# Kernel tuning notes

Measured on AMD Instinct MI355X. Metric: run time of the kernel, lower is better.

## Reference

```python
import jax, jax.numpy as jnp
import numpy as np

B, M, T, R, N_IN, O, K = 2, 20000, 8, 5, 64, 128, 4  # batch, verts, N_theta, N_rho, in, out, kernels


def setup_inputs() -> dict:
    key = jax.random.key(0)
    k1, k2, k3, k4 = jax.random.split(key, 4)
    signal = jax.random.normal(k1, (B, M, N_IN), dtype=jnp.float32)
    u = jax.random.uniform(k2, (B, M, T, R, 3), dtype=jnp.float32, minval=1e-3, maxval=1.0)
    bary_weights = u / jnp.sum(u, axis=-1, keepdims=True)  # barycentric: sum to 1
    bary_indices = jax.random.randint(k3, (B, M, T, R, 3), 0, M, dtype=jnp.int32)
    # glorot-ish scale for (amt_kernel, N_theta, N_rho, out, in) weight tensor
    kernel = jax.random.normal(k4, (K, T, R, O, N_IN), dtype=jnp.float32) * 0.05
    return {"signal": signal, "bary_weights": bary_weights,
            "bary_indices": bary_indices, "kernel": kernel}


def reference(signal, bary_weights, bary_indices, kernel):
    # signal: (B, m, n); bary_weights/indices: (B, m, T, R, 3); kernel: (K, T, R, o, n)
    Ksum = jnp.sum(kernel, axis=0)                      # sum over kernels k: (T, R, o, n)
    T_ = kernel.shape[1]
    j = jnp.arange(T_)
    rot = (j[None, :] + j[:, None]) % T_                # rot[r, j] = (j + r) % T
    Krot = Ksum[rot]                                    # (T_r, T_j, R, o, n)

    def one(sig, w, idx):
        g = sig[idx]                                    # gather: (m, T, R, 3, n)
        x = jnp.einsum('mtrc,mtrcn->mtrn', w, g)        # barycentric pullback (m, T, R, n)
        conv = jnp.einsum('rjion,mjin->rmo', Krot, x)   # per-rotation conv (T_r, m, o)
        a = jax.nn.relu(conv)
        norms = jnp.linalg.norm(a, axis=-1)             # (T_r, m)
        best = jnp.argmax(norms, axis=0)                # (m,)
        return jnp.take_along_axis(a, best[None, :, None], axis=0)[0]  # angular max pool (m, o)

    return jax.vmap(one)(signal, bary_weights, bary_indices)
```

## Files before the change

### kernel.cpp

```cpp
#include <hip/hip_runtime.h>
#include <hip/hip_bf16.h>


typedef _Float16 f16;
typedef _Float16 f16x8 __attribute__((ext_vector_type(8)));
typedef float f32x4 __attribute__((ext_vector_type(4)));

#define B_   2
#define M_   20000
#define T_   8
#define R_   5
#define NIN  64
#define O_   128
#define K_   4

#define PTS   (B_*M_)
#define KSEG  2560
#define KPHY  5120
#define KLOG  7680
#define NQ    1024
#define SCALE 16.0f
#define INVSS (1.0f/(SCALE*SCALE))

#define BM    64
#define BK    32
#define TS    (KLOG/BK)

__global__ void k_ksum(const float* __restrict__ kern, float* __restrict__ ksum) {
    int i = blockIdx.x * 256 + threadIdx.x;
    const int total = T_ * R_ * O_ * NIN;
    if (i >= total) return;
    float s = 0.f;
#pragma unroll
    for (int k = 0; k < K_; k++) s += kern[k * total + i];
    ksum[i] = s;
}

__global__ void k_wt(const float* __restrict__ ksum, f16* __restrict__ wt) {
    int idx = blockIdx.x * 256 + threadIdx.x;
    const int total = NQ * KSEG;
    if (idx >= total) return;
    int q = idx / KSEG;
    int k = idx - q * KSEG;
    int r = q >> 7, o = q & 127;
    int j = k / 320;
    int rem = k - j * 320;
    int i = rem >> 6, n = rem & 63;
    int t = (j + r) & 7;
    float v = SCALE * ksum[((((t * R_ + i) * O_ + o) << 6) + n)];
    f16 hi = (f16)v;
    f16 lo = (f16)(v - (float)hi);
    f16* row = wt + (size_t)q * KLOG;
    row[k] = hi;
    row[k + KSEG] = hi;
    row[k + 2 * KSEG] = lo;
}

__global__ void k_interp(const float* __restrict__ sig, const float* __restrict__ bw,
                         const int* __restrict__ bi, f16* __restrict__ X,
                         int pt0, int rows_pad) {
    int nwaves = gridDim.x * 4;
    int wav = (blockIdx.x * 256 + threadIdx.x) >> 6;
    int lane = threadIdx.x & 63;
    int ntask = rows_pad * T_;
    for (int task = wav; task < ntask; task += nwaves) {
        int lr = task >> 3;
        int j = task & 7;
        int pt = pt0 + lr;
        f16* rowp = X + (size_t)lr * KPHY + j * 320;
        if (pt >= PTS) {
#pragma unroll
            for (int i = 0; i < R_; i++) {
                rowp[i * 64 + lane] = (f16)0.f;
                rowp[KSEG + i * 64 + lane] = (f16)0.f;
            }
            continue;
        }
        int b = (pt >= M_) ? 1 : 0;
        const float* sb = sig + (size_t)b * M_ * NIN;
        size_t base = (size_t)pt * 120 + j * 15;
        float wv = 0.f;
        int iv = 0;
        if (lane < 15) { wv = bw[base + lane]; iv = bi[base + lane]; }
#pragma unroll
        for (int i = 0; i < R_; i++) {
            float w0 = __shfl(wv, i * 3 + 0, 64);
            float w1 = __shfl(wv, i * 3 + 1, 64);
            float w2 = __shfl(wv, i * 3 + 2, 64);
            int i0 = __shfl(iv, i * 3 + 0, 64);
            int i1 = __shfl(iv, i * 3 + 1, 64);
            int i2 = __shfl(iv, i * 3 + 2, 64);
            float x = w0 * sb[(size_t)i0 * NIN + lane];
            x = fmaf(w1, sb[(size_t)i1 * NIN + lane], x);
            x = fmaf(w2, sb[(size_t)i2 * NIN + lane], x);
            x *= SCALE;
            f16 hi = (f16)x;
            f16 lo = (f16)(x - (float)hi);
            rowp[i * 64 + lane] = hi;
            rowp[KSEG + i * 64 + lane] = lo;
        }
    }
}

__global__ __launch_bounds__(512, 2) void k_gemm_fused(
    const f16* __restrict__ X, const f16* __restrict__ WT,
    float* __restrict__ out, int pt0) {
    __shared__ __align__(16) f16 As[2][64 * 32];
    __shared__ __align__(16) f16 Bs[2][1024 * 32];
    __shared__ float sred[8][64];
    const int m0 = blockIdx.x * BM;
    const int t = threadIdx.x;
    const int w = t >> 6, lane = t & 63;
    const int wr = w >> 2, wc = w & 3;
    const int lq = lane >> 4, lr16 = lane & 15;
    const int flane = (lr16 >> 1) & 3;
    const int src_off = (((lane & 3) ^ ((lane >> 3) & 3)) << 3);

    f32x4 acc[2][16];
#pragma unroll
    for (int a = 0; a < 2; a++)
#pragma unroll
        for (int b = 0; b < 16; b++) acc[a][b] = (f32x4){0.f, 0.f, 0.f, 0.f};

    const f16* pA = X + (size_t)(m0 + 8 * w + ((lane & 31) >> 2)) * KPHY + src_off;
    const f16* pB = WT + (size_t)(w * 128 + (lane >> 2)) * KLOG + src_off;

#define STAGE(S, BUF) do {                                                                \
        int k0_ = (S) * BK;                                                               \
        int kA_ = k0_ - ((k0_ >= KPHY) ? KPHY : 0);               \
        if (lane < 32)                                                                    \
            __builtin_amdgcn_global_load_lds(                                             \
                (const __attribute__((address_space(1))) void*)(pA + kA_),                \
                (__attribute__((address_space(3))) void*)(&As[BUF][w * 256 + (lane & 31) * 8]), \
                16, 0, 0);                                                                \
        _Pragma("unroll")                                                                 \
        for (int i_ = 0; i_ < 8; i_++)                                                    \
            __builtin_amdgcn_global_load_lds(                                             \
                (const __attribute__((address_space(1))) void*)(pB + i_ * 16 * KLOG + k0_), \
                (__attribute__((address_space(3))) void*)(&Bs[BUF][(w * 8 + i_) * 512 + lane * 8]), \
                16, 0, 0);                                                                \
    } while (0)

    STAGE(0, 0);

    for (int s = 0; s < TS; ++s) {
        int cur = s & 1;
        if (s + 1 < TS) {
            STAGE(s + 1, cur ^ 1);
            asm volatile("s_waitcnt vmcnt(9)" ::: "memory");
        } else {
            asm volatile("s_waitcnt vmcnt(0)" ::: "memory");
        }
        __builtin_amdgcn_s_barrier();
        __builtin_amdgcn_sched_barrier(0);

        const f16* Ac = &As[cur][0];
        const f16* Bc = &Bs[cur][0];
        const int cho = (lq ^ flane) << 3;
        f16x8 af0 = *(const f16x8*)(Ac + (wr * 32 + lr16) * 32 + cho);
        f16x8 af1 = *(const f16x8*)(Ac + (wr * 32 + 16 + lr16) * 32 + cho);
#pragma unroll
        for (int nf = 0; nf < 16; nf++) {
            f16x8 bf = *(const f16x8*)(Bc + (wc * 256 + nf * 16 + lr16) * 32 + cho);
            acc[0][nf] = __builtin_amdgcn_mfma_f32_16x16x32_f16(af0, bf, acc[0][nf], 0, 0, 0);
            acc[1][nf] = __builtin_amdgcn_mfma_f32_16x16x32_f16(af1, bf, acc[1][nf], 0, 0, 0);
        }
        __builtin_amdgcn_sched_barrier(0);
        __builtin_amdgcn_s_barrier();
    }
#undef STAGE

#pragma unroll
    for (int mf = 0; mf < 2; mf++)
#pragma unroll
        for (int nf = 0; nf < 16; nf++)
#pragma unroll
            for (int jj = 0; jj < 4; jj++)
                acc[mf][nf][jj] = fmaxf(acc[mf][nf][jj], 0.f);

#pragma unroll
    for (int mf = 0; mf < 2; mf++)
#pragma unroll
        for (int jj = 0; jj < 4; jj++)
#pragma unroll
            for (int half = 0; half < 2; half++) {
                float s = 0.f;
#pragma unroll
                for (int nf2 = 0; nf2 < 8; nf2++) {
                    float v = acc[mf][half * 8 + nf2][jj];
                    s = fmaf(v, v, s);
                }
                s += __shfl_xor(s, 1, 64);
                s += __shfl_xor(s, 2, 64);
                s += __shfl_xor(s, 4, 64);
                s += __shfl_xor(s, 8, 64);
                if (lr16 == 0) sred[wc * 2 + half][wr * 32 + mf * 16 + lq * 4 + jj] = s;
            }
    __syncthreads();

#pragma unroll
    for (int mf = 0; mf < 2; mf++)
#pragma unroll
        for (int jj = 0; jj < 4; jj++) {
            int row = wr * 32 + mf * 16 + lq * 4 + jj;
            float bs = sred[0][row];
            int br = 0;
#pragma unroll
            for (int r = 1; r < 8; r++) {
                float v = sred[r][row];
                if (v > bs) { bs = v; br = r; }
            }
            int pt = pt0 + m0 + row;
            if ((br >> 1) == wc && pt < PTS) {
                float* op = out + (size_t)pt * O_ + lr16;
                if (br & 1) {
#pragma unroll
                    for (int nf2 = 0; nf2 < 8; nf2++) op[nf2 * 16] = acc[mf][8 + nf2][jj] * INVSS;
                } else {
#pragma unroll
                    for (int nf2 = 0; nf2 < 8; nf2++) op[nf2 * 16] = acc[mf][nf2][jj] * INVSS;
                }
            }
        }
}

extern "C" void kernel_launch(void* const* d_in, const int* in_sizes, int n_in,
                              void* d_out, int out_size, void* d_ws, size_t ws_size,
                              hipStream_t stream) {
    const float* sig = (const float*)d_in[0];
    const float* bw = (const float*)d_in[1];
    const int* bi = (const int*)d_in[2];
    const float* kern = (const float*)d_in[3];
    float* out = (float*)d_out;
    char* ws = (char*)d_ws;

    const size_t sz_ksum = (size_t)T_ * R_ * O_ * NIN * sizeof(float);
    const size_t sz_wt = (size_t)NQ * KLOG * sizeof(f16);
    float* ksum = (float*)ws;
    f16* WT = (f16*)(ws + sz_ksum);
    f16* X = (f16*)(ws + sz_ksum + sz_wt);

    size_t persist = sz_ksum + sz_wt;
    size_t avail = (ws_size > persist) ? (ws_size - persist) : 0;
    long maxrows = (long)(avail / ((size_t)KPHY * sizeof(f16)));
    int chunk = (int)((maxrows / BM) * BM);
    if (chunk < BM) chunk = BM;
    const int PTS_PAD = ((PTS + BM - 1) / BM) * BM;
    if (chunk > PTS_PAD) chunk = PTS_PAD;

    k_ksum<<<(T_ * R_ * O_ * NIN + 255) / 256, 256, 0, stream>>>(kern, ksum);
    k_wt<<<(NQ * KSEG + 255) / 256, 256, 0, stream>>>(ksum, WT);

    for (int pt0 = 0; pt0 < PTS; pt0 += chunk) {
        int rem = PTS - pt0;
        int rows = (rem < chunk) ? rem : chunk;
        int rows_pad = (rows + BM - 1) & ~(BM - 1);
        k_interp<<<2048, 256, 0, stream>>>(sig, bw, bi, X, pt0, rows_pad);
        k_gemm_fused<<<rows_pad / BM, 512, 0, stream>>>(X, WT, out, pt0);
    }
}
```

Measured before the change: 1.650 ms.

## Retile GEMM to 256x256 blocks with XCD remap and separate select pass

The fused GEMM previously used 64-row blocks that each covered all 1024 rotation-output columns. It now uses 256x256 tiles with BK=64 and an XCD-aware block remapping. Conv results and per-rotation-pair norms go to global memory, and a new k_select kernel does the argmax and pooled write. This raises arithmetic intensity and reuse of the shared weight operand, at the cost of an extra fp32 conv buffer round-trip and one more launch. The interp kernel also replaces shuffle broadcasts with wave-uniform scalar loads.

```diff
diff --git a/kernel.cpp b/kernel.cpp
--- a/kernel.cpp
+++ b/kernel.cpp
@@ -15,6 +15,7 @@
 #define K_   4
 
 #define PTS   (B_*M_)
+#define PTSPAD 40192
 #define KSEG  2560
 #define KPHY  5120
 #define KLOG  7680
@@ -22,8 +23,8 @@
 #define SCALE 16.0f
 #define INVSS (1.0f/(SCALE*SCALE))
 
-#define BM    64
-#define BK    32
+#define BM    256
+#define BK    64
 #define TS    (KLOG/BK)
 
 __global__ void k_ksum(const float* __restrict__ kern, float* __restrict__ ksum) {
@@ -64,8 +65,9 @@
     int lane = threadIdx.x & 63;
     int ntask = rows_pad * T_;
     for (int task = wav; task < ntask; task += nwaves) {
-        int lr = task >> 3;
-        int j = task & 7;
+        int tu = __builtin_amdgcn_readfirstlane(task);
+        int lr = tu >> 3;
+        int j = tu & 7;
         int pt = pt0 + lr;
         f16* rowp = X + (size_t)lr * KPHY + j * 320;
         if (pt >= PTS) {
@@ -78,18 +80,12 @@
         }
         int b = (pt >= M_) ? 1 : 0;
         const float* sb = sig + (size_t)b * M_ * NIN;
-        size_t base = (size_t)pt * 120 + j * 15;
-        float wv = 0.f;
-        int iv = 0;
-        if (lane < 15) { wv = bw[base + lane]; iv = bi[base + lane]; }
+        const float* wp = bw + (size_t)pt * 120 + j * 15;
+        const int* ip = bi + (size_t)pt * 120 + j * 15;
 #pragma unroll
         for (int i = 0; i < R_; i++) {
-            float w0 = __shfl(wv, i * 3 + 0, 64);
-            float w1 = __shfl(wv, i * 3 + 1, 64);
-            float w2 = __shfl(wv, i * 3 + 2, 64);
-            int i0 = __shfl(iv, i * 3 + 0, 64);
-            int i1 = __shfl(iv, i * 3 + 1, 64);
-            int i2 = __shfl(iv, i * 3 + 2, 64);
+            float w0 = wp[i * 3], w1 = wp[i * 3 + 1], w2 = wp[i * 3 + 2];
+            int i0 = ip[i * 3], i1 = ip[i * 3 + 1], i2 = ip[i * 3 + 2];
             float x = w0 * sb[(size_t)i0 * NIN + lane];
             x = fmaf(w1, sb[(size_t)i1 * NIN + lane], x);
             x = fmaf(w2, sb[(size_t)i2 * NIN + lane], x);
@@ -102,43 +98,50 @@
     }
 }
 
-__global__ __launch_bounds__(512, 2) void k_gemm_fused(
+__global__ __launch_bounds__(512, 1) void k_gemm(
     const f16* __restrict__ X, const f16* __restrict__ WT,
-    float* __restrict__ out, int pt0) {
-    __shared__ __align__(16) f16 As[2][64 * 32];
-    __shared__ __align__(16) f16 Bs[2][1024 * 32];
-    __shared__ float sred[8][64];
-    const int m0 = blockIdx.x * BM;
+    float* __restrict__ conv, float* __restrict__ norms, int pt0) {
+    __shared__ __align__(16) f16 As[2][256 * 64];
+    __shared__ __align__(16) f16 Bs[2][256 * 64];
+    __shared__ float sred[4][256];
+
+    int nwg = gridDim.x;
+    int bq = nwg >> 3, br_ = nwg & 7;
+    int xcd = blockIdx.x & 7, slot = blockIdx.x >> 3;
+    int logical = (xcd < br_ ? xcd * (bq + 1) : br_ * (bq + 1) + (xcd - br_) * bq) + slot;
+    int mblk = logical >> 2, nb = logical & 3;
+    const int m0 = mblk * BM;
+    const int n0 = nb * 256;
+
     const int t = threadIdx.x;
     const int w = t >> 6, lane = t & 63;
     const int wr = w >> 2, wc = w & 3;
     const int lq = lane >> 4, lr16 = lane & 15;
-    const int flane = (lr16 >> 1) & 3;
-    const int src_off = (((lane & 3) ^ ((lane >> 3) & 3)) << 3);
-
-    f32x4 acc[2][16];
-#pragma unroll
-    for (int a = 0; a < 2; a++)
-#pragma unroll
-        for (int b = 0; b < 16; b++) acc[a][b] = (f32x4){0.f, 0.f, 0.f, 0.f};
-
-    const f16* pA = X + (size_t)(m0 + 8 * w + ((lane & 31) >> 2)) * KPHY + src_off;
-    const f16* pB = WT + (size_t)(w * 128 + (lane >> 2)) * KLOG + src_off;
-
-#define STAGE(S, BUF) do {                                                                \
-        int k0_ = (S) * BK;                                                               \
-        int kA_ = k0_ - ((k0_ >= KPHY) ? KPHY : 0);               \
-        if (lane < 32)                                                                    \
-            __builtin_amdgcn_global_load_lds(                                             \
-                (const __attribute__((address_space(1))) void*)(pA + kA_),                \
-                (__attribute__((address_space(3))) void*)(&As[BUF][w * 256 + (lane & 31) * 8]), \
-                16, 0, 0);                                                                \
-        _Pragma("unroll")                                                                 \
-        for (int i_ = 0; i_ < 8; i_++)                                                    \
-            __builtin_amdgcn_global_load_lds(                                             \
-                (const __attribute__((address_space(1))) void*)(pB + i_ * 16 * KLOG + k0_), \
-                (__attribute__((address_space(3))) void*)(&Bs[BUF][(w * 8 + i_) * 512 + lane * 8]), \
-                16, 0, 0);                                                                \
+    const int fr = lr16 & 7;
+    const int src_off = (((t & 7) ^ ((t >> 3) & 7)) << 3);
+
+    f32x4 acc[8][4];
+#pragma unroll
+    for (int a = 0; a < 8; a++)
+#pragma unroll
+        for (int b = 0; b < 4; b++) acc[a][b] = (f32x4){0.f, 0.f, 0.f, 0.f};
+
+    const f16* pA = X + (size_t)(m0 + (t >> 3)) * KPHY + src_off;
+    const f16* pB = WT + (size_t)(n0 + (t >> 3)) * KLOG + src_off;
+
+#define STAGE(S, BUF) do {                                                            \
+        int k0_ = (S) * BK;                                                           \
+        int kA_ = k0_ - ((k0_ >= KPHY) ? KPHY : 0);           \
+        _Pragma("unroll")                                                             \
+        for (int i_ = 0; i_ < 4; i_++)                                                \
+            __builtin_amdgcn_global_load_lds(                                         \
+                (const __attribute__((address_space(1))) void*)(pA + kA_ + (size_t)i_ * 64 * KPHY), \
+                (__attribute__((address_space(3))) void*)(&As[BUF][t * 8 + i_ * 4096]), 16, 0, 0); \
+        _Pragma("unroll")                                                             \
+        for (int i_ = 0; i_ < 4; i_++)                                                \
+            __builtin_amdgcn_global_load_lds(                                         \
+                (const __attribute__((address_space(1))) void*)(pB + k0_ + (size_t)i_ * 64 * KLOG), \
+                (__attribute__((address_space(3))) void*)(&Bs[BUF][t * 8 + i_ * 4096]), 16, 0, 0); \
     } while (0)
 
     STAGE(0, 0);
@@ -147,7 +150,7 @@
         int cur = s & 1;
         if (s + 1 < TS) {
             STAGE(s + 1, cur ^ 1);
-            asm volatile("s_waitcnt vmcnt(9)" ::: "memory");
+            asm volatile("s_waitcnt vmcnt(8)" ::: "memory");
         } else {
             asm volatile("s_waitcnt vmcnt(0)" ::: "memory");
         }
@@ -156,14 +159,21 @@
 
         const f16* Ac = &As[cur][0];
         const f16* Bc = &Bs[cur][0];
-        const int cho = (lq ^ flane) << 3;
-        f16x8 af0 = *(const f16x8*)(Ac + (wr * 32 + lr16) * 32 + cho);
-        f16x8 af1 = *(const f16x8*)(Ac + (wr * 32 + 16 + lr16) * 32 + cho);
-#pragma unroll
-        for (int nf = 0; nf < 16; nf++) {
-            f16x8 bf = *(const f16x8*)(Bc + (wc * 256 + nf * 16 + lr16) * 32 + cho);
-            acc[0][nf] = __builtin_amdgcn_mfma_f32_16x16x32_f16(af0, bf, acc[0][nf], 0, 0, 0);
-            acc[1][nf] = __builtin_amdgcn_mfma_f32_16x16x32_f16(af1, bf, acc[1][nf], 0, 0, 0);
+#pragma unroll
+        for (int kk = 0; kk < 2; ++kk) {
+            const int cho = ((kk * 4 + lq) ^ fr) << 3;
+            f16x8 af[8], bf[4];
+#pragma unroll
+            for (int mf = 0; mf < 8; mf++)
+                af[mf] = *(const f16x8*)(Ac + (wr * 128 + mf * 16 + lr16) * 64 + cho);
+#pragma unroll
+            for (int nf = 0; nf < 4; nf++)
+                bf[nf] = *(const f16x8*)(Bc + (wc * 64 + nf * 16 + lr16) * 64 + cho);
+#pragma unroll
+            for (int mf = 0; mf < 8; mf++)
+#pragma unroll
+                for (int nf = 0; nf < 4; nf++)
+                    acc[mf][nf] = __builtin_amdgcn_mfma_f32_16x16x32_f16(af[mf], bf[nf], acc[mf][nf], 0, 0, 0);
         }
         __builtin_amdgcn_sched_barrier(0);
         __builtin_amdgcn_s_barrier();
@@ -171,57 +181,63 @@
 #undef STAGE
 
 #pragma unroll
-    for (int mf = 0; mf < 2; mf++)
-#pragma unroll
-        for (int nf = 0; nf < 16; nf++)
+    for (int mf = 0; mf < 8; mf++)
+#pragma unroll
+        for (int nf = 0; nf < 4; nf++)
 #pragma unroll
             for (int jj = 0; jj < 4; jj++)
                 acc[mf][nf][jj] = fmaxf(acc[mf][nf][jj], 0.f);
 
 #pragma unroll
-    for (int mf = 0; mf < 2; mf++)
-#pragma unroll
-        for (int jj = 0; jj < 4; jj++)
-#pragma unroll
-            for (int half = 0; half < 2; half++) {
-                float s = 0.f;
-#pragma unroll
-                for (int nf2 = 0; nf2 < 8; nf2++) {
-                    float v = acc[mf][half * 8 + nf2][jj];
-                    s = fmaf(v, v, s);
-                }
-                s += __shfl_xor(s, 1, 64);
-                s += __shfl_xor(s, 2, 64);
-                s += __shfl_xor(s, 4, 64);
-                s += __shfl_xor(s, 8, 64);
-                if (lr16 == 0) sred[wc * 2 + half][wr * 32 + mf * 16 + lq * 4 + jj] = s;
+    for (int mf = 0; mf < 8; mf++)
+#pragma unroll
+        for (int jj = 0; jj < 4; jj++) {
+            int rowl = wr * 128 + mf * 16 + lq * 4 + jj;
+            float s = 0.f;
+#pragma unroll
+            for (int nf = 0; nf < 4; nf++) {
+                float v = acc[mf][nf][jj];
+                s = fmaf(v, v, s);
+                conv[(size_t)(m0 + rowl) * NQ + n0 + wc * 64 + nf * 16 + lr16] = v;
             }
+            s += __shfl_xor(s, 1, 64);
+            s += __shfl_xor(s, 2, 64);
+            s += __shfl_xor(s, 4, 64);
+            s += __shfl_xor(s, 8, 64);
+            if (lr16 == 0) sred[wc][rowl] = s;
+        }
     __syncthreads();
-
-#pragma unroll
-    for (int mf = 0; mf < 2; mf++)
-#pragma unroll
-        for (int jj = 0; jj < 4; jj++) {
-            int row = wr * 32 + mf * 16 + lq * 4 + jj;
-            float bs = sred[0][row];
-            int br = 0;
-#pragma unroll
-            for (int r = 1; r < 8; r++) {
-                float v = sred[r][row];
-                if (v > bs) { bs = v; br = r; }
-            }
-            int pt = pt0 + m0 + row;
-            if ((br >> 1) == wc && pt < PTS) {
-                float* op = out + (size_t)pt * O_ + lr16;
-                if (br & 1) {
-#pragma unroll
-                    for (int nf2 = 0; nf2 < 8; nf2++) op[nf2 * 16] = acc[mf][8 + nf2][jj] * INVSS;
-                } else {
-#pragma unroll
-                    for (int nf2 = 0; nf2 < 8; nf2++) op[nf2 * 16] = acc[mf][nf2][jj] * INVSS;
-                }
-            }
-        }
+    if (t < 256) {
+        float e = sred[0][t] + sred[1][t];
+        float o = sred[2][t] + sred[3][t];
+        float2* np = (float2*)&norms[(size_t)(pt0 + m0 + t) * 8 + nb * 2];
+        *np = make_float2(e, o);
+    }
+}
+
+__global__ void k_select(const float* __restrict__ conv, const float* __restrict__ norms,
+                         float* __restrict__ out, int pt0, int rows) {
+    int nwaves = gridDim.x * 4;
+    int wav = (blockIdx.x * 256 + threadIdx.x) >> 6;
+    int lane = threadIdx.x & 63;
+    for (int task = wav; task < rows; task += nwaves) {
+        int tu = __builtin_amdgcn_readfirstlane(task);
+        int pt = pt0 + tu;
+        if (pt >= PTS) continue;
+        const float* np = norms + (size_t)pt * 8;
+        float bs = np[0];
+        int br = 0;
+#pragma unroll
+        for (int r = 1; r < 8; r++) {
+            float v = np[r];
+            if (v > bs) { bs = v; br = r; }
+        }
+        const float2 v = *(const float2*)&conv[(size_t)tu * NQ + br * 128 + lane * 2];
+        float2 o;
+        o.x = v.x * INVSS;
+        o.y = v.y * INVSS;
+        *(float2*)&out[(size_t)pt * O_ + lane * 2] = o;
+    }
 }
 
 extern "C" void kernel_launch(void* const* d_in, const int* in_sizes, int n_in,
@@ -236,17 +252,21 @@
 
     const size_t sz_ksum = (size_t)T_ * R_ * O_ * NIN * sizeof(float);
     const size_t sz_wt = (size_t)NQ * KLOG * sizeof(f16);
+    const size_t sz_norms = (size_t)PTSPAD * 8 * sizeof(float);
     float* ksum = (float*)ws;
     f16* WT = (f16*)(ws + sz_ksum);
-    f16* X = (f16*)(ws + sz_ksum + sz_wt);
-
-    size_t persist = sz_ksum + sz_wt;
+    float* norms = (float*)(ws + sz_ksum + sz_wt);
+    char* dyn = ws + sz_ksum + sz_wt + sz_norms;
+
+    size_t persist = sz_ksum + sz_wt + sz_norms;
     size_t avail = (ws_size > persist) ? (ws_size - persist) : 0;
-    long maxrows = (long)(avail / ((size_t)KPHY * sizeof(f16)));
+    long maxrows = (long)(avail / (size_t)(KPHY * 2 + NQ * 4));
     int chunk = (int)((maxrows / BM) * BM);
     if (chunk < BM) chunk = BM;
-    const int PTS_PAD = ((PTS + BM - 1) / BM) * BM;
-    if (chunk > PTS_PAD) chunk = PTS_PAD;
+    if (chunk > PTSPAD) chunk = PTSPAD;
+
+    f16* X = (f16*)dyn;
+    float* conv = (float*)(dyn + (size_t)chunk * KPHY * sizeof(f16));
 
     k_ksum<<<(T_ * R_ * O_ * NIN + 255) / 256, 256, 0, stream>>>(kern, ksum);
     k_wt<<<(NQ * KSEG + 255) / 256, 256, 0, stream>>>(ksum, WT);
@@ -255,7 +275,8 @@
         int rem = PTS - pt0;
         int rows = (rem < chunk) ? rem : chunk;
         int rows_pad = (rows + BM - 1) & ~(BM - 1);
-        k_interp<<<2048, 256, 0, stream>>>(sig, bw, bi, X, pt0, rows_pad);
-        k_gemm_fused<<<rows_pad / BM, 512, 0, stream>>>(X, WT, out, pt0);
-    }
-}
+        k_interp<<<4096, 256, 0, stream>>>(sig, bw, bi, X, pt0, rows_pad);
+        k_gemm<<<(rows_pad / BM) * 4, 512, 0, stream>>>(X, WT, conv, norms, pt0);
+        k_select<<<2048, 256, 0, stream>>>(conv, norms, out, pt0, rows);
+    }
+}
```

After: 1.457 ms. -11.7%, faster.
